# Optimization experiments

Hardware: AMD Instinct MI355X
Metric: run time of the kernel (lower is better)

The kernel has to match this reference:

```python
import jax, jax.numpy as jnp
import numpy as np
import math

N_HEADS = 8

def _bn_eval(x, g, b, m, v):
    # eval-mode BatchNorm over the last (query_size) axis, eps=1e-5 (torch default)
    return g * (x - m) * jax.lax.rsqrt(v + 1e-5) + b

def _forward(ht, k_proj_W, query, uk_W, u_q1W, u_q2, vhq, vhk, vcq, vck,
             k_proj_b, q_b, u_q1b, bnc_g, bnc_b, bnc_m, bnc_v, bnk_g, bnk_b, bnk_m, bnk_v):
    B, T, C = ht.shape
    N = N_HEADS
    D = C // N
    Q = k_proj_W.shape[-1]
    # contextual key: per-head [mean, std] over time (torch.std is unbiased)
    mean = jnp.mean(ht, axis=1)
    std = jnp.std(ht, axis=1, ddof=1)
    # cat on dim=2 of [B,C,1] then reshape -> interleaved [m0,s0,m1,s1,...]
    c = jnp.concatenate([mean[..., None], std[..., None]], axis=2).reshape(B, N, 2 * D)
    head_ck = jnp.einsum('bkl,klm->bkm', c, uk_W)                           # [B,N,Q]
    head_key = jnp.einsum('btkl,klm->btkm', ht.reshape(B, T, N, D), k_proj_W)  # [B,T,N,Q]
    value = ht.reshape(B, T, N, D)
    # contextual query
    cq = jnp.einsum('bkl,klm->bkm', c, u_q1W) + u_q1b                       # [B,N,Q]
    cq = jnp.tanh(_bn_eval(jax.nn.relu(cq), bnc_g, bnc_b, bnc_m, bnc_v))
    cq = jnp.einsum('bkm,kmn->bkn', cq, u_q2)                               # [B,N,A]
    # lambda gates
    lam_k = jax.nn.sigmoid(
        jnp.einsum('btkq,kq->btk', head_key, vhk[..., 0])
        + jnp.einsum('bkq,kq->bk', head_ck, vck[..., 0])[:, None, :]
    )[..., None]                                                            # [B,T,N,1]
    lam_q = jax.nn.sigmoid(
        jnp.einsum('kqa,kaq->k', query, vhq[..., 0])[None, :]
        + jnp.einsum('bka,kaq->bk', cq, vcq[..., 0])
    )[:, :, None, None]                                                     # [B,N,1,1]
    head_cq = (1.0 - lam_q) * query[None] + lam_q * cq[:, :, None, :]       # [B,N,Q,A]
    head_key = (1.0 - lam_k) * head_key + lam_k * head_ck[:, None]          # [B,T,N,Q]
    head_key = jnp.tanh(_bn_eval(jax.nn.relu(head_key + k_proj_b), bnk_g, bnk_b, bnk_m, bnk_v))
    scores = jnp.einsum('btkq,bkqa->btka', head_key, head_cq) / math.sqrt(Q) + q_b  # [B,T,N,A]
    p = jax.nn.softmax(scores, axis=1)                                      # softmax over time
    mu = jnp.sum(value * p, axis=1)                                         # [B,N,D] (A==D)
    rh = jnp.sqrt(jnp.clip(jnp.sum(value * value * p, axis=1) - mu * mu, 1e-9, None))
    return jnp.concatenate([mu, rh], axis=1).reshape(B, -1)                 # [B, 2*C]


def setup_inputs() -> dict:
    B, T, C = 16, 2000, 1536
    N, D, Q, A = 8, 192, 256, 192
    key = jax.random.key(0)
    ks = jax.random.split(key, 24)

    def xav(k, shape):
        fan = shape[-2] + shape[-1] if len(shape) >= 2 else shape[-1] + 1
        return jax.random.normal(k, shape, jnp.float32) * float(np.sqrt(2.0 / fan))

    return {
        'ht': jax.random.normal(ks[0], (B, T, C), jnp.float32),
        'k_proj_W': xav(ks[1], (N, D, Q)),
        'query': xav(ks[2], (N, Q, A)),
        'uk_W': xav(ks[3], (N, 2 * D, Q)),
        'u_q1W': xav(ks[4], (N, 2 * D, Q)),
        'u_q2': xav(ks[5], (N, Q, A)),
        'vhq': xav(ks[6], (N, A, Q, 1)),
        'vhk': xav(ks[7], (N, Q, 1)),
        'vcq': xav(ks[8], (N, A, Q, 1)),
        'vck': xav(ks[9], (N, Q, 1)),
        'k_proj_b': xav(ks[10], (N, Q)),
        'q_b': xav(ks[11], (N, A)),
        'u_q1b': xav(ks[12], (N, Q)),
        'bnc_g': jax.random.normal(ks[13], (Q,), jnp.float32) * 0.1 + 1.0,
        'bnc_b': jax.random.normal(ks[14], (Q,), jnp.float32) * 0.1,
        'bnc_m': jax.random.normal(ks[15], (Q,), jnp.float32) * 0.1,
        'bnc_v': jax.random.uniform(ks[16], (Q,), jnp.float32, 0.5, 1.5),
        'bnk_g': jax.random.normal(ks[17], (Q,), jnp.float32) * 0.1 + 1.0,
        'bnk_b': jax.random.normal(ks[18], (Q,), jnp.float32) * 0.1,
        'bnk_m': jax.random.normal(ks[19], (Q,), jnp.float32) * 0.1,
        'bnk_v': jax.random.uniform(ks[20], (Q,), jnp.float32, 0.5, 1.5),
    }


def reference(ht, k_proj_W, query, uk_W, u_q1W, u_q2, vhq, vhk, vcq, vck,
              k_proj_b, q_b, u_q1b, bnc_g, bnc_b, bnc_m, bnc_v, bnk_g, bnk_b, bnk_m, bnk_v):
    return _forward(ht, k_proj_W, query, uk_W, u_q1W, u_q2, vhq, vhk, vcq, vck,
                    k_proj_b, q_b, u_q1b, bnc_g, bnc_b, bnc_m, bnc_v,
                    bnk_g, bnk_b, bnk_m, bnk_v)
```

## Files before the change

kernel.cpp:

```cpp
#include <hip/hip_runtime.h>
#include <math.h>

#define BB 16
#define TT 2000
#define CC 1536
#define NH 8
#define DD 192
#define QQ 256
#define AA 192

#define WS_PSUM   0u
#define WS_PSQ    614400u
#define WS_CVEC   1228800u
#define WS_HCK    1277952u
#define WS_CKDOT  1310720u
#define WS_W1T    1310848u
#define WS_HCQT   1507456u
#define WS_PART   4653184u

#define LDS_BYTES 54272

typedef short bf16x8 __attribute__((ext_vector_type(8)));
typedef float f32x4  __attribute__((ext_vector_type(4)));

__device__ __forceinline__ float fast_tanh(float x) {
    return 1.f - 2.f / (__expf(2.f * x) + 1.f);
}
__device__ __forceinline__ float fast_sigmoid(float x) {
    return 1.f / (1.f + __expf(-x));
}
__device__ __forceinline__ short f2bf(float x) {
    unsigned u = __builtin_bit_cast(unsigned, x);
    u += 0x7FFFu + ((u >> 16) & 1u);
    return (short)(u >> 16);
}

__global__ void k_stats(const float* __restrict__ ht, float* __restrict__ ws) {
    int bid = blockIdx.x;
    int tc = bid % 25;
    int b  = bid / 25;
    int c4 = threadIdx.x * 4;
    const float* p = ht + ((size_t)b * TT + (size_t)tc * 80) * CC + c4;
    float4 s  = make_float4(0.f, 0.f, 0.f, 0.f);
    float4 s2 = make_float4(0.f, 0.f, 0.f, 0.f);
    #pragma unroll 8
    for (int i = 0; i < 80; ++i) {
        float4 v = *(const float4*)(p + (size_t)i * CC);
        s.x += v.x; s.y += v.y; s.z += v.z; s.w += v.w;
        s2.x = fmaf(v.x, v.x, s2.x); s2.y = fmaf(v.y, v.y, s2.y);
        s2.z = fmaf(v.z, v.z, s2.z); s2.w = fmaf(v.w, v.w, s2.w);
    }
    *(float4*)(ws + WS_PSUM + (size_t)(tc * BB + b) * CC + c4) = s;
    *(float4*)(ws + WS_PSQ  + (size_t)(tc * BB + b) * CC + c4) = s2;
}

__global__ void k_finstats(float* __restrict__ ws) {
    int b  = blockIdx.x;
    int c4 = threadIdx.x * 4;
    float4 s  = make_float4(0.f, 0.f, 0.f, 0.f);
    float4 s2 = make_float4(0.f, 0.f, 0.f, 0.f);
    for (int tc = 0; tc < 25; ++tc) {
        float4 a = *(const float4*)(ws + WS_PSUM + (size_t)(tc * BB + b) * CC + c4);
        float4 q = *(const float4*)(ws + WS_PSQ  + (size_t)(tc * BB + b) * CC + c4);
        s.x += a.x; s.y += a.y; s.z += a.z; s.w += a.w;
        s2.x += q.x; s2.y += q.y; s2.z += q.z; s2.w += q.w;
    }
    float mean[4] = {s.x, s.y, s.z, s.w};
    float sq[4]   = {s2.x, s2.y, s2.z, s2.w};
    float sd[4];
    #pragma unroll
    for (int j = 0; j < 4; ++j) {
        float m = mean[j] * (1.f / TT);
        float var = (sq[j] - (float)TT * m * m) * (1.f / (TT - 1));
        mean[j] = m;
        sd[j] = sqrtf(fmaxf(var, 0.f));
    }
    int k = c4 / DD, dd = c4 - k * DD;
    float* dst = ws + WS_CVEC + (size_t)b * 3072 + k * 384 + 2 * dd;
    *(float4*)(dst)     = make_float4(mean[0], sd[0], mean[1], sd[1]);
    *(float4*)(dst + 4) = make_float4(mean[2], sd[2], mean[3], sd[3]);
}

__global__ void k_convw(const float* __restrict__ kpW, float* __restrict__ ws) {
    int k  = blockIdx.x / 3, dc = blockIdx.x % 3;
    int q  = threadIdx.x;
    short* dst = (short*)(ws + WS_W1T) + ((size_t)k * QQ + q) * DD;
    const float* src = kpW + (size_t)k * DD * QQ + q;
    #pragma unroll 4
    for (int u = 0; u < 16; ++u) {
        int d = dc * 64 + u * 4;
        short4 s4;
        s4.x = f2bf(src[(size_t)(d + 0) * QQ]);
        s4.y = f2bf(src[(size_t)(d + 1) * QQ]);
        s4.z = f2bf(src[(size_t)(d + 2) * QQ]);
        s4.w = f2bf(src[(size_t)(d + 3) * QQ]);
        *(short4*)(dst + d) = s4;
    }
}

__global__ void k_prep(const float* __restrict__ ukW,  const float* __restrict__ uq1W,
                       const float* __restrict__ uq1b, const float* __restrict__ uq2,
                       const float* __restrict__ query, const float* __restrict__ vhq,
                       const float* __restrict__ vcq,  const float* __restrict__ vck,
                       const float* __restrict__ bncg, const float* __restrict__ bncb,
                       const float* __restrict__ bncm, const float* __restrict__ bncv,
                       float* __restrict__ ws) {
    __shared__ float cv[384];
    __shared__ float cqh[QQ];
    __shared__ float cq2s[AA];
    __shared__ float red[256];
    int bid = blockIdx.x;
    int b = bid >> 3, k = bid & 7;
    int tid = threadIdx.x;

    for (int i = tid; i < 384; i += 256)
        cv[i] = ws[WS_CVEC + (size_t)b * 3072 + k * 384 + i];
    __syncthreads();

    int q = tid;
    const float* up = ukW + (size_t)k * 384 * QQ;
    float hck = 0.f;
    for (int l = 0; l < 384; ++l) hck = fmaf(cv[l], up[l * QQ + q], hck);
    ws[WS_HCK + (size_t)(b * NH + k) * QQ + q] = hck;

    const float* u1 = uq1W + (size_t)k * 384 * QQ;
    float cq = uq1b[k * QQ + q];
    for (int l = 0; l < 384; ++l) cq = fmaf(cv[l], u1[l * QQ + q], cq);
    cq = fmaxf(cq, 0.f);
    float sc = bncg[q] * rsqrtf(bncv[q] + 1e-5f);
    cq = fast_tanh(fmaf(cq - bncm[q], sc, bncb[q]));
    cqh[q] = cq;

    red[tid] = hck * vck[k * QQ + q];
    __syncthreads();
    #pragma unroll
    for (int off = 128; off > 0; off >>= 1) {
        if (tid < off) red[tid] += red[tid + off];
        __syncthreads();
    }
    if (tid == 0) ws[WS_CKDOT + b * NH + k] = red[0];
    __syncthreads();

    float c2 = 0.f;
    if (tid < AA) {
        const float* u2 = uq2 + (size_t)k * QQ * AA + tid;
        for (int m = 0; m < QQ; ++m) c2 = fmaf(cqh[m], u2[m * AA], c2);
        cq2s[tid] = c2;
    }

    float part = 0.f;
    for (int idx = tid; idx < QQ * AA; idx += 256) {
        int qq = idx / AA, aa = idx - qq * AA;
        part = fmaf(query[(size_t)k * QQ * AA + idx],
                    vhq[(size_t)k * AA * QQ + aa * QQ + qq], part);
    }
    if (tid < AA) {
        const float* vq = vcq + (size_t)k * AA * QQ + (size_t)tid * QQ;
        float w = 0.f;
        for (int qx = 0; qx < QQ; ++qx) w += vq[qx];
        part = fmaf(c2, w, part);
    }
    red[tid] = part;
    __syncthreads();
    #pragma unroll
    for (int off = 128; off > 0; off >>= 1) {
        if (tid < off) red[tid] += red[tid + off];
        __syncthreads();
    }
    float lq = fast_sigmoid(red[0]);

    short* hq = (short*)(ws + WS_HCQT) + (size_t)(b * NH + k) * AA * QQ;
    const float* qr = query + (size_t)k * QQ * AA;
    for (int pos = tid; pos < AA * QQ; pos += 256) {
        int aa = pos >> 8, qq = pos & 255;
        float val = (1.f - lq) * qr[qq * AA + aa] + lq * cq2s[aa];
        hq[pos] = f2bf(val);
    }
}

__global__ __launch_bounds__(256, 3) void k_main(
        const float* __restrict__ ht,   const float* __restrict__ kpb,
        const float* __restrict__ vhk,  const float* __restrict__ qb_,
        const float* __restrict__ bnkg, const float* __restrict__ bnkb,
        const float* __restrict__ bnkm, const float* __restrict__ bnkv,
        float* __restrict__ ws) {
    extern __shared__ char lds[];
    float4* tbl4   = (float4*)(lds + 32768);
    float*  lamred = (float*)(lds + 36864);
    char*   Ab     = lds + 37888;
    float*  S_ld   = (float*)lds;

    int bid = blockIdx.x;
    int bk = bid >> 5, tile = bid & 31;
    int b = bk >> 3, k = bk & 7;
    int t0 = tile * 64;
    int tid = threadIdx.x;
    int w  = tid >> 6;
    int l  = tid & 63;
    int lr = l & 15, lg = l >> 4;
    int nv = min(64, TT - t0);

    {
        int q = tid;
        float hckv = ws[WS_HCK + (size_t)bk * QQ + q];
        float kbv  = kpb[k * QQ + q];
        float bscv = bnkg[q] * rsqrtf(bnkv[q] + 1e-5f);
        float bshv = bnkb[q] - bnkm[q] * bscv;
        tbl4[q] = make_float4(hckv, kbv, bscv, bshv);
    }
    float ckd = ws[WS_CKDOT + bk];

    float vv[4];
    #pragma unroll
    for (int cc = 0; cc < 4; ++cc)
        vv[cc] = vhk[k * QQ + w * 64 + cc * 16 + lr];

    f32x4 acc1[4][4];
    #pragma unroll
    for (int tg = 0; tg < 4; ++tg)
        #pragma unroll
        for (int cc = 0; cc < 4; ++cc) acc1[tg][cc] = (f32x4){0.f, 0.f, 0.f, 0.f};

    const short* w1s = (const short*)(ws + WS_W1T) + (size_t)k * QQ * DD;
    const int r_ = tid >> 2, cs = tid & 3;

    #pragma unroll
    for (int half = 0; half < 2; ++half) {
        __syncthreads();
        {
            const float* src = ht + ((size_t)b * TT + t0 + r_) * CC + k * DD + half * 96;
            bool ok = (t0 + r_) < TT;
            #pragma unroll
            for (int u = 0; u < 6; ++u) {
                int c4 = cs * 24 + u * 4;
                float4 v = make_float4(0.f, 0.f, 0.f, 0.f);
                if (ok) v = *(const float4*)(src + c4);
                short4 s4;
                s4.x = f2bf(v.x); s4.y = f2bf(v.y); s4.z = f2bf(v.z); s4.w = f2bf(v.w);
                int byte = (r_ << 8) + (c4 << 1);
                byte ^= (r_ & 7) << 4;
                *(short4*)(Ab + byte) = s4;
            }
        }
        __syncthreads();
        bf16x8 af[4][3];
        #pragma unroll
        for (int tg = 0; tg < 4; ++tg)
            #pragma unroll
            for (int kb = 0; kb < 3; ++kb) {
                int t = tg * 16 + lr;
                int byte = (t << 8) + ((kb * 32 + lg * 8) << 1);
                byte ^= (t & 7) << 4;
                af[tg][kb] = *(const bf16x8*)(Ab + byte);
            }
        #pragma unroll
        for (int cc = 0; cc < 4; ++cc) {
            const short* bq = w1s + (size_t)(w * 64 + cc * 16 + lr) * DD + half * 96 + lg * 8;
            bf16x8 bf0 = *(const bf16x8*)(bq);
            bf16x8 bf1 = *(const bf16x8*)(bq + 32);
            bf16x8 bf2 = *(const bf16x8*)(bq + 64);
            #pragma unroll
            for (int tg = 0; tg < 4; ++tg) {
                acc1[tg][cc] = __builtin_amdgcn_mfma_f32_16x16x32_bf16(af[tg][0], bf0, acc1[tg][cc], 0, 0, 0);
                acc1[tg][cc] = __builtin_amdgcn_mfma_f32_16x16x32_bf16(af[tg][1], bf1, acc1[tg][cc], 0, 0, 0);
                acc1[tg][cc] = __builtin_amdgcn_mfma_f32_16x16x32_bf16(af[tg][2], bf2, acc1[tg][cc], 0, 0, 0);
            }
        }
    }

    {
        float rdp[4][4];
        #pragma unroll
        for (int tg = 0; tg < 4; ++tg)
            #pragma unroll
            for (int r = 0; r < 4; ++r) {
                float s = 0.f;
                #pragma unroll
                for (int cc = 0; cc < 4; ++cc) s = fmaf(acc1[tg][cc][r], vv[cc], s);
                #pragma unroll
                for (int off = 1; off < 16; off <<= 1) s += __shfl_xor(s, off);
                rdp[tg][r] = s;
            }
        if (lr == 0) {
            #pragma unroll
            for (int tg = 0; tg < 4; ++tg)
                #pragma unroll
                for (int r = 0; r < 4; ++r)
                    lamred[w * 64 + tg * 16 + lg * 4 + r] = rdp[tg][r];
        }
    }
    __syncthreads();
    if (tid < 64) {
        float s = lamred[tid] + lamred[64 + tid] + lamred[128 + tid] + lamred[192 + tid];
        lamred[tid] = fast_sigmoid(s + ckd);
    }
    __syncthreads();

    {
        float lamv[4][4];
        #pragma unroll
        for (int tg = 0; tg < 4; ++tg)
            #pragma unroll
            for (int r = 0; r < 4; ++r)
                lamv[tg][r] = lamred[tg * 16 + lg * 4 + r];
        #pragma unroll
        for (int cc = 0; cc < 4; ++cc) {
            int q = w * 64 + cc * 16 + lr;
            float4 tv = tbl4[q];
            #pragma unroll
            for (int tg = 0; tg < 4; ++tg)
                #pragma unroll
                for (int r = 0; r < 4; ++r) {
                    float lam = lamv[tg][r];
                    float hk = (1.f - lam) * acc1[tg][cc][r] + lam * tv.x;
                    float x  = fmaxf(hk + tv.y, 0.f);
                    float kh = fast_tanh(fmaf(x, tv.z, tv.w));
                    int t = tg * 16 + lg * 4 + r;
                    int byte = (t << 9) + (q << 1);
                    byte ^= (t & 7) << 4;
                    *(short*)(lds + byte) = f2bf(kh);
                }
        }
    }
    __syncthreads();

    f32x4 acc2[4][3];
    #pragma unroll
    for (int tg = 0; tg < 4; ++tg)
        #pragma unroll
        for (int cc = 0; cc < 3; ++cc) acc2[tg][cc] = (f32x4){0.f, 0.f, 0.f, 0.f};

    const short* hq = (const short*)(ws + WS_HCQT) + (size_t)bk * AA * QQ;
    #pragma unroll
    for (int kb = 0; kb < 8; ++kb) {
        bf16x8 kf[4];
        #pragma unroll
        for (int tg = 0; tg < 4; ++tg) {
            int t = tg * 16 + lr;
            int byte = (t << 9) + ((kb * 32 + lg * 8) << 1);
            byte ^= (t & 7) << 4;
            kf[tg] = *(const bf16x8*)(lds + byte);
        }
        #pragma unroll
        for (int cc = 0; cc < 3; ++cc) {
            const short* ba = hq + (size_t)(w * 48 + cc * 16 + lr) * QQ + kb * 32 + lg * 8;
            bf16x8 bfv = *(const bf16x8*)ba;
            #pragma unroll
            for (int tg = 0; tg < 4; ++tg)
                acc2[tg][cc] = __builtin_amdgcn_mfma_f32_16x16x32_bf16(kf[tg], bfv, acc2[tg][cc], 0, 0, 0);
        }
    }
    __syncthreads();

    #pragma unroll
    for (int tg = 0; tg < 4; ++tg)
        #pragma unroll
        for (int cc = 0; cc < 3; ++cc) {
            int a = w * 48 + cc * 16 + lr;
            #pragma unroll
            for (int r = 0; r < 4; ++r)
                S_ld[(tg * 16 + lg * 4 + r) * 196 + a] = acc2[tg][cc][r];
        }
    __syncthreads();

    if (tid < AA) {
        int a = tid;
        float qb = qb_[k * AA + a];
        const float* vp = ht + ((size_t)b * TT + t0) * CC + k * DD + a;
        float lsum = 0.f, mac = 0.f, m2 = 0.f;
        if (nv == 64) {
            #pragma unroll 8
            for (int t = 0; t < 64; ++t) {
                float s = fminf(fmaf(S_ld[t * 196 + a], 0.0625f, qb), 30.f);
                float e = __expf(s);
                float v = vp[(size_t)t * CC];
                float t1 = e * v;
                lsum += e;
                mac  += t1;
                m2    = fmaf(t1, v, m2);
            }
        } else {
            for (int t = 0; t < nv; ++t) {
                float s = fminf(fmaf(S_ld[t * 196 + a], 0.0625f, qb), 30.f);
                float e = __expf(s);
                float v = vp[(size_t)t * CC];
                float t1 = e * v;
                lsum += e;
                mac  += t1;
                m2    = fmaf(t1, v, m2);
            }
        }
        ((float4*)(ws + WS_PART))[(size_t)(bk * 32 + tile) * AA + a] =
            make_float4(0.f, lsum, mac, m2);
    }
}

__global__ void k_merge(const float* __restrict__ ws, float* __restrict__ out) {
    int bk = blockIdx.x;
    int b = bk >> 3, k = bk & 7;
    int a = threadIdx.x;
    const float4* part = (const float4*)(ws + WS_PART) + (size_t)bk * 32 * AA + a;
    float M = -3.0e38f;
    #pragma unroll 4
    for (int ti = 0; ti < 32; ++ti) M = fmaxf(M, part[(size_t)ti * AA].x);
    float L = 0.f, MU = 0.f, M2 = 0.f;
    #pragma unroll 4
    for (int ti = 0; ti < 32; ++ti) {
        float4 p = part[(size_t)ti * AA];
        float sc = __expf(p.x - M);
        L  = fmaf(p.y, sc, L);
        MU = fmaf(p.z, sc, MU);
        M2 = fmaf(p.w, sc, M2);
    }
    MU /= L;
    M2 /= L;
    float rh = sqrtf(fmaxf(M2 - MU * MU, 1e-9f));
    out[(size_t)b * 3072 + k * DD + a]      = MU;
    out[(size_t)b * 3072 + CC + k * DD + a] = rh;
}

extern "C" void kernel_launch(void* const* d_in, const int* in_sizes, int n_in,
                              void* d_out, int out_size, void* d_ws, size_t ws_size,
                              hipStream_t stream) {
    const float* ht    = (const float*)d_in[0];
    const float* kpW   = (const float*)d_in[1];
    const float* query = (const float*)d_in[2];
    const float* ukW   = (const float*)d_in[3];
    const float* uq1W  = (const float*)d_in[4];
    const float* uq2   = (const float*)d_in[5];
    const float* vhq   = (const float*)d_in[6];
    const float* vhk   = (const float*)d_in[7];
    const float* vcq   = (const float*)d_in[8];
    const float* vck   = (const float*)d_in[9];
    const float* kpb   = (const float*)d_in[10];
    const float* qb    = (const float*)d_in[11];
    const float* uq1b  = (const float*)d_in[12];
    const float* bncg  = (const float*)d_in[13];
    const float* bncb  = (const float*)d_in[14];
    const float* bncm  = (const float*)d_in[15];
    const float* bncv  = (const float*)d_in[16];
    const float* bnkg  = (const float*)d_in[17];
    const float* bnkb  = (const float*)d_in[18];
    const float* bnkm  = (const float*)d_in[19];
    const float* bnkv  = (const float*)d_in[20];
    float* ws  = (float*)d_ws;
    float* out = (float*)d_out;

    hipFuncSetAttribute(reinterpret_cast<const void*>(k_main),
                        hipFuncAttributeMaxDynamicSharedMemorySize, LDS_BYTES);

    k_stats   <<<400, 384, 0, stream>>>(ht, ws);
    k_finstats<<<16, 384, 0, stream>>>(ws);
    k_convw   <<<24, 256, 0, stream>>>(kpW, ws);
    k_prep    <<<128, 256, 0, stream>>>(ukW, uq1W, uq1b, uq2, query, vhq, vcq, vck,
                                        bncg, bncb, bncm, bncv, ws);
    k_main    <<<4096, 256, LDS_BYTES, stream>>>(ht, kpb, vhk, qb,
                                                 bnkg, bnkb, bnkm, bnkv, ws);
    k_merge   <<<128, 192, 0, stream>>>(ws, out);
}
```

Baseline: 675.3 us.

## Fuse prep kernels, pre-swizzle MFMA operands, and run softmax epilogue from registers

Merges the stats, weight conversion and batch-independent query-dot work into one launch, and folds finstats into k_prep. Weight and head-query operands are stored in an MFMA fragment-ready layout so k_main can load them contiguously per lane. The score epilogue now reads the accumulators directly instead of staging scores through LDS, which cuts LDS to allow 4 blocks per CU. k_merge drops the unused max-rescale pass. The combined changes add code complexity and register pressure in k_main.

Result: faster. 598.8 us (-11.3%).

```diff
diff --git a/kernel.cpp b/kernel.cpp
--- a/kernel.cpp
+++ b/kernel.cpp
@@ -11,14 +11,15 @@
 
 #define WS_PSUM   0u
 #define WS_PSQ    614400u
-#define WS_CVEC   1228800u
-#define WS_HCK    1277952u
-#define WS_CKDOT  1310720u
-#define WS_W1T    1310848u
-#define WS_HCQT   1507456u
-#define WS_PART   4653184u
-
-#define LDS_BYTES 54272
+#define WS_HCK    1228800u
+#define WS_CKDOT  1261568u
+#define WS_W1T    1261696u
+#define WS_HCQT   1458304u
+#define WS_PART   4604032u
+#define WS_QVHQ   7749760u
+#define WS_VCQS   7749768u
+
+#define LDS_BYTES 37888
 
 typedef short bf16x8 __attribute__((ext_vector_type(8)));
 typedef float f32x4  __attribute__((ext_vector_type(4)));
@@ -35,97 +36,117 @@
     return (short)(u >> 16);
 }
 
-__global__ void k_stats(const float* __restrict__ ht, float* __restrict__ ws) {
-    int bid = blockIdx.x;
-    int tc = bid % 25;
-    int b  = bid / 25;
-    int c4 = threadIdx.x * 4;
-    const float* p = ht + ((size_t)b * TT + (size_t)tc * 80) * CC + c4;
-    float4 s  = make_float4(0.f, 0.f, 0.f, 0.f);
-    float4 s2 = make_float4(0.f, 0.f, 0.f, 0.f);
-    #pragma unroll 8
-    for (int i = 0; i < 80; ++i) {
-        float4 v = *(const float4*)(p + (size_t)i * CC);
-        s.x += v.x; s.y += v.y; s.z += v.z; s.w += v.w;
-        s2.x = fmaf(v.x, v.x, s2.x); s2.y = fmaf(v.y, v.y, s2.y);
-        s2.z = fmaf(v.z, v.z, s2.z); s2.w = fmaf(v.w, v.w, s2.w);
-    }
-    *(float4*)(ws + WS_PSUM + (size_t)(tc * BB + b) * CC + c4) = s;
-    *(float4*)(ws + WS_PSQ  + (size_t)(tc * BB + b) * CC + c4) = s2;
-}
-
-__global__ void k_finstats(float* __restrict__ ws) {
-    int b  = blockIdx.x;
-    int c4 = threadIdx.x * 4;
-    float4 s  = make_float4(0.f, 0.f, 0.f, 0.f);
-    float4 s2 = make_float4(0.f, 0.f, 0.f, 0.f);
-    for (int tc = 0; tc < 25; ++tc) {
-        float4 a = *(const float4*)(ws + WS_PSUM + (size_t)(tc * BB + b) * CC + c4);
-        float4 q = *(const float4*)(ws + WS_PSQ  + (size_t)(tc * BB + b) * CC + c4);
-        s.x += a.x; s.y += a.y; s.z += a.z; s.w += a.w;
-        s2.x += q.x; s2.y += q.y; s2.z += q.z; s2.w += q.w;
-    }
-    float mean[4] = {s.x, s.y, s.z, s.w};
-    float sq[4]   = {s2.x, s2.y, s2.z, s2.w};
-    float sd[4];
-    #pragma unroll
-    for (int j = 0; j < 4; ++j) {
-        float m = mean[j] * (1.f / TT);
-        float var = (sq[j] - (float)TT * m * m) * (1.f / (TT - 1));
-        mean[j] = m;
-        sd[j] = sqrtf(fmaxf(var, 0.f));
-    }
-    int k = c4 / DD, dd = c4 - k * DD;
-    float* dst = ws + WS_CVEC + (size_t)b * 3072 + k * 384 + 2 * dd;
-    *(float4*)(dst)     = make_float4(mean[0], sd[0], mean[1], sd[1]);
-    *(float4*)(dst + 4) = make_float4(mean[2], sd[2], mean[3], sd[3]);
-}
-
-__global__ void k_convw(const float* __restrict__ kpW, float* __restrict__ ws) {
-    int k  = blockIdx.x / 3, dc = blockIdx.x % 3;
-    int q  = threadIdx.x;
-    short* dst = (short*)(ws + WS_W1T) + ((size_t)k * QQ + q) * DD;
-    const float* src = kpW + (size_t)k * DD * QQ + q;
-    #pragma unroll 4
-    for (int u = 0; u < 16; ++u) {
-        int d = dc * 64 + u * 4;
-        short4 s4;
-        s4.x = f2bf(src[(size_t)(d + 0) * QQ]);
-        s4.y = f2bf(src[(size_t)(d + 1) * QQ]);
-        s4.z = f2bf(src[(size_t)(d + 2) * QQ]);
-        s4.w = f2bf(src[(size_t)(d + 3) * QQ]);
-        *(short4*)(dst + d) = s4;
+__global__ void k_pre(const float* __restrict__ ht,   const float* __restrict__ kpW,
+                      const float* __restrict__ query, const float* __restrict__ vhq,
+                      const float* __restrict__ vcq,  float* __restrict__ ws) {
+    int bid = blockIdx.x, tid = threadIdx.x;
+    if (bid < 400) {
+        int tc = bid % 25;
+        int b  = bid / 25;
+        int c4 = tid * 4;
+        const float* p = ht + ((size_t)b * TT + (size_t)tc * 80) * CC + c4;
+        float4 s  = make_float4(0.f, 0.f, 0.f, 0.f);
+        float4 s2 = make_float4(0.f, 0.f, 0.f, 0.f);
+        #pragma unroll 8
+        for (int i = 0; i < 80; ++i) {
+            float4 v = *(const float4*)(p + (size_t)i * CC);
+            s.x += v.x; s.y += v.y; s.z += v.z; s.w += v.w;
+            s2.x = fmaf(v.x, v.x, s2.x); s2.y = fmaf(v.y, v.y, s2.y);
+            s2.z = fmaf(v.z, v.z, s2.z); s2.w = fmaf(v.w, v.w, s2.w);
+        }
+        *(float4*)(ws + WS_PSUM + (size_t)(tc * BB + b) * CC + c4) = s;
+        *(float4*)(ws + WS_PSQ  + (size_t)(tc * BB + b) * CC + c4) = s2;
+    } else if (bid < 448) {
+        if (tid < 256) {
+            int kk  = (bid - 400) / 6, kbg = (bid - 400) % 6;
+            int qg  = tid >> 4, lr = tid & 15;
+            short* w1f = (short*)(ws + WS_W1T) + (size_t)kk * 49152;
+            const float* src = kpW + (size_t)kk * DD * QQ;
+            int q = qg * 16 + lr;
+            #pragma unroll
+            for (int lg = 0; lg < 4; ++lg) {
+                bf16x8 v8;
+                #pragma unroll
+                for (int e = 0; e < 8; ++e) {
+                    int d = kbg * 32 + lg * 8 + e;
+                    v8[e] = f2bf(src[(size_t)d * QQ + q]);
+                }
+                *(bf16x8*)(w1f + ((qg * 6 + kbg) * 512 + (lg * 16 + lr) * 8)) = v8;
+            }
+        }
+    } else {
+        int kk = bid - 448;
+        __shared__ float red6[6];
+        float qv = 0.f;
+        if (tid < 192) {
+            int aa = tid;
+            const float* qp = query + (size_t)kk * QQ * AA + aa;
+            const float* hp = vhq + (size_t)kk * AA * QQ + (size_t)aa * QQ;
+            const float* cp = vcq + (size_t)kk * AA * QQ + (size_t)aa * QQ;
+            float vs = 0.f;
+            #pragma unroll 4
+            for (int qq = 0; qq < QQ; ++qq) {
+                qv = fmaf(qp[(size_t)qq * AA], hp[qq], qv);
+                vs += cp[qq];
+            }
+            ws[WS_VCQS + kk * 192 + aa] = vs;
+        }
+        #pragma unroll
+        for (int off = 1; off < 64; off <<= 1) qv += __shfl_xor(qv, off);
+        if ((tid & 63) == 0) red6[tid >> 6] = qv;
+        __syncthreads();
+        if (tid == 0)
+            ws[WS_QVHQ + kk] = red6[0] + red6[1] + red6[2] + red6[3] + red6[4] + red6[5];
     }
 }
 
 __global__ void k_prep(const float* __restrict__ ukW,  const float* __restrict__ uq1W,
                        const float* __restrict__ uq1b, const float* __restrict__ uq2,
-                       const float* __restrict__ query, const float* __restrict__ vhq,
-                       const float* __restrict__ vcq,  const float* __restrict__ vck,
+                       const float* __restrict__ query, const float* __restrict__ vck,
                        const float* __restrict__ bncg, const float* __restrict__ bncb,
                        const float* __restrict__ bncm, const float* __restrict__ bncv,
                        float* __restrict__ ws) {
     __shared__ float cv[384];
     __shared__ float cqh[QQ];
-    __shared__ float cq2s[AA];
     __shared__ float red[256];
+    __shared__ float stage[32 * 196];
     int bid = blockIdx.x;
     int b = bid >> 3, k = bid & 7;
     int tid = threadIdx.x;
 
-    for (int i = tid; i < 384; i += 256)
-        cv[i] = ws[WS_CVEC + (size_t)b * 3072 + k * 384 + i];
+    if (tid < 192) {
+        float s = 0.f, s2 = 0.f;
+        #pragma unroll 5
+        for (int tc = 0; tc < 25; ++tc) {
+            s  += ws[WS_PSUM + (size_t)(tc * BB + b) * CC + k * DD + tid];
+            s2 += ws[WS_PSQ  + (size_t)(tc * BB + b) * CC + k * DD + tid];
+        }
+        float mean = s * (1.f / TT);
+        float var  = (s2 - (float)TT * mean * mean) * (1.f / (TT - 1));
+        cv[2 * tid]     = mean;
+        cv[2 * tid + 1] = sqrtf(fmaxf(var, 0.f));
+    }
     __syncthreads();
 
     int q = tid;
     const float* up = ukW + (size_t)k * 384 * QQ;
-    float hck = 0.f;
-    for (int l = 0; l < 384; ++l) hck = fmaf(cv[l], up[l * QQ + q], hck);
+    float hck = 0.f, hckb = 0.f;
+    #pragma unroll 4
+    for (int l = 0; l < 384; l += 2) {
+        hck  = fmaf(cv[l],     up[l * QQ + q],       hck);
+        hckb = fmaf(cv[l + 1], up[(l + 1) * QQ + q], hckb);
+    }
+    hck += hckb;
     ws[WS_HCK + (size_t)(b * NH + k) * QQ + q] = hck;
 
     const float* u1 = uq1W + (size_t)k * 384 * QQ;
-    float cq = uq1b[k * QQ + q];
-    for (int l = 0; l < 384; ++l) cq = fmaf(cv[l], u1[l * QQ + q], cq);
+    float cq = uq1b[k * QQ + q], cqb = 0.f;
+    #pragma unroll 4
+    for (int l = 0; l < 384; l += 2) {
+        cq  = fmaf(cv[l],     u1[l * QQ + q],       cq);
+        cqb = fmaf(cv[l + 1], u1[(l + 1) * QQ + q], cqb);
+    }
+    cq += cqb;
     cq = fmaxf(cq, 0.f);
     float sc = bncg[q] * rsqrtf(bncv[q] + 1e-5f);
     cq = fast_tanh(fmaf(cq - bncm[q], sc, bncb[q]));
@@ -144,41 +165,46 @@
     float c2 = 0.f;
     if (tid < AA) {
         const float* u2 = uq2 + (size_t)k * QQ * AA + tid;
+        #pragma unroll 4
         for (int m = 0; m < QQ; ++m) c2 = fmaf(cqh[m], u2[m * AA], c2);
-        cq2s[tid] = c2;
-    }
-
-    float part = 0.f;
-    for (int idx = tid; idx < QQ * AA; idx += 256) {
-        int qq = idx / AA, aa = idx - qq * AA;
-        part = fmaf(query[(size_t)k * QQ * AA + idx],
-                    vhq[(size_t)k * AA * QQ + aa * QQ + qq], part);
-    }
-    if (tid < AA) {
-        const float* vq = vcq + (size_t)k * AA * QQ + (size_t)tid * QQ;
-        float w = 0.f;
-        for (int qx = 0; qx < QQ; ++qx) w += vq[qx];
-        part = fmaf(c2, w, part);
-    }
-    red[tid] = part;
+    }
+
+    red[tid] = (tid < AA) ? c2 * ws[WS_VCQS + k * 192 + tid] : 0.f;
     __syncthreads();
     #pragma unroll
     for (int off = 128; off > 0; off >>= 1) {
         if (tid < off) red[tid] += red[tid + off];
         __syncthreads();
     }
-    float lq = fast_sigmoid(red[0]);
-
-    short* hq = (short*)(ws + WS_HCQT) + (size_t)(b * NH + k) * AA * QQ;
-    const float* qr = query + (size_t)k * QQ * AA;
-    for (int pos = tid; pos < AA * QQ; pos += 256) {
-        int aa = pos >> 8, qq = pos & 255;
-        float val = (1.f - lq) * qr[qq * AA + aa] + lq * cq2s[aa];
-        hq[pos] = f2bf(val);
-    }
-}
-
-__global__ __launch_bounds__(256, 3) void k_main(
+    float lq = fast_sigmoid(red[0] + ws[WS_QVHQ + k]);
+    float one_lq = 1.f - lq;
+
+    {
+        const float* qpan = query + (size_t)k * QQ * AA;
+        short* hqf = (short*)(ws + WS_HCQT) + (size_t)(b * NH + k) * 49152;
+        int ag = tid >> 4, lr = tid & 15;
+        for (int kb = 0; kb < 8; ++kb) {
+            __syncthreads();
+            for (int i = tid; i < 32 * 192; i += 256) {
+                int qt = i / 192, aa = i - qt * 192;
+                stage[qt * 196 + aa] = qpan[(size_t)(kb * 32 + qt) * AA + aa];
+            }
+            __syncthreads();
+            if (tid < AA) {
+                #pragma unroll
+                for (int lg = 0; lg < 4; ++lg) {
+                    bf16x8 v8;
+                    #pragma unroll
+                    for (int e = 0; e < 8; ++e)
+                        v8[e] = f2bf(fmaf(one_lq, stage[(lg * 8 + e) * 196 + tid], lq * c2));
+                    *(bf16x8*)(hqf + ((ag * 8 + kb) * 64 + lg * 16 + lr) * 8) = v8;
+                }
+            }
+        }
+    }
+}
+
+__global__ __launch_bounds__(256, 4) void k_main(
         const float* __restrict__ ht,   const float* __restrict__ kpb,
         const float* __restrict__ vhk,  const float* __restrict__ qb_,
         const float* __restrict__ bnkg, const float* __restrict__ bnkb,
@@ -187,17 +213,16 @@
     extern __shared__ char lds[];
     float4* tbl4   = (float4*)(lds + 32768);
     float*  lamred = (float*)(lds + 36864);
-    char*   Ab     = lds + 37888;
-    float*  S_ld   = (float*)lds;
+    char*   Ab     = lds;
 
     int bid = blockIdx.x;
     int bk = bid >> 5, tile = bid & 31;
     int b = bk >> 3, k = bk & 7;
     int t0 = tile * 64;
     int tid = threadIdx.x;
-    int w  = tid >> 6;
-    int l  = tid & 63;
-    int lr = l & 15, lg = l >> 4;
+    int w   = tid >> 6;
+    int lid = tid & 63;
+    int lr = lid & 15, lg = lid >> 4;
     int nv = min(64, TT - t0);
 
     {
@@ -209,7 +234,6 @@
         tbl4[q] = make_float4(hckv, kbv, bscv, bshv);
     }
     float ckd = ws[WS_CKDOT + bk];
-
     float vv[4];
     #pragma unroll
     for (int cc = 0; cc < 4; ++cc)
@@ -221,7 +245,7 @@
         #pragma unroll
         for (int cc = 0; cc < 4; ++cc) acc1[tg][cc] = (f32x4){0.f, 0.f, 0.f, 0.f};
 
-    const short* w1s = (const short*)(ws + WS_W1T) + (size_t)k * QQ * DD;
+    const short* w1f = (const short*)(ws + WS_W1T) + (size_t)k * 49152;
     const int r_ = tid >> 2, cs = tid & 3;
 
     #pragma unroll
@@ -243,28 +267,25 @@
             }
         }
         __syncthreads();
-        bf16x8 af[4][3];
-        #pragma unroll
-        for (int tg = 0; tg < 4; ++tg)
-            #pragma unroll
-            for (int kb = 0; kb < 3; ++kb) {
+        #pragma unroll
+        for (int kb = 0; kb < 3; ++kb) {
+            bf16x8 af[4];
+            #pragma unroll
+            for (int tg = 0; tg < 4; ++tg) {
                 int t = tg * 16 + lr;
                 int byte = (t << 8) + ((kb * 32 + lg * 8) << 1);
                 byte ^= (t & 7) << 4;
-                af[tg][kb] = *(const bf16x8*)(Ab + byte);
-            }
-        #pragma unroll
-        for (int cc = 0; cc < 4; ++cc) {
-            const short* bq = w1s + (size_t)(w * 64 + cc * 16 + lr) * DD + half * 96 + lg * 8;
-            bf16x8 bf0 = *(const bf16x8*)(bq);
-            bf16x8 bf1 = *(const bf16x8*)(bq + 32);
-            bf16x8 bf2 = *(const bf16x8*)(bq + 64);
-            #pragma unroll
-            for (int tg = 0; tg < 4; ++tg) {
-                acc1[tg][cc] = __builtin_amdgcn_mfma_f32_16x16x32_bf16(af[tg][0], bf0, acc1[tg][cc], 0, 0, 0);
-                acc1[tg][cc] = __builtin_amdgcn_mfma_f32_16x16x32_bf16(af[tg][1], bf1, acc1[tg][cc], 0, 0, 0);
-                acc1[tg][cc] = __builtin_amdgcn_mfma_f32_16x16x32_bf16(af[tg][2], bf2, acc1[tg][cc], 0, 0, 0);
-            }
+                af[tg] = *(const bf16x8*)(Ab + byte);
+            }
+            bf16x8 bf4[4];
+            #pragma unroll
+            for (int cc = 0; cc < 4; ++cc)
+                bf4[cc] = *(const bf16x8*)(w1f + (((w * 4 + cc) * 6 + half * 3 + kb) << 9) + (lid << 3));
+            #pragma unroll
+            for (int cc = 0; cc < 4; ++cc)
+                #pragma unroll
+                for (int tg = 0; tg < 4; ++tg)
+                    acc1[tg][cc] = __builtin_amdgcn_mfma_f32_16x16x32_bf16(af[tg], bf4[cc], acc1[tg][cc], 0, 0, 0);
         }
     }
 
@@ -330,7 +351,7 @@
         #pragma unroll
         for (int cc = 0; cc < 3; ++cc) acc2[tg][cc] = (f32x4){0.f, 0.f, 0.f, 0.f};
 
-    const short* hq = (const short*)(ws + WS_HCQT) + (size_t)bk * AA * QQ;
+    const short* hqf = (const short*)(ws + WS_HCQT) + (size_t)bk * 49152;
     #pragma unroll
     for (int kb = 0; kb < 8; ++kb) {
         bf16x8 kf[4];
@@ -341,57 +362,60 @@
             byte ^= (t & 7) << 4;
             kf[tg] = *(const bf16x8*)(lds + byte);
         }
-        #pragma unroll
-        for (int cc = 0; cc < 3; ++cc) {
-            const short* ba = hq + (size_t)(w * 48 + cc * 16 + lr) * QQ + kb * 32 + lg * 8;
-            bf16x8 bfv = *(const bf16x8*)ba;
+        bf16x8 bf3[3];
+        #pragma unroll
+        for (int cc = 0; cc < 3; ++cc)
+            bf3[cc] = *(const bf16x8*)(hqf + (((w * 3 + cc) * 8 + kb) << 9) + (lid << 3));
+        #pragma unroll
+        for (int cc = 0; cc < 3; ++cc)
             #pragma unroll
             for (int tg = 0; tg < 4; ++tg)
-                acc2[tg][cc] = __builtin_amdgcn_mfma_f32_16x16x32_bf16(kf[tg], bfv, acc2[tg][cc], 0, 0, 0);
-        }
-    }
-    __syncthreads();
-
-    #pragma unroll
-    for (int tg = 0; tg < 4; ++tg)
-        #pragma unroll
-        for (int cc = 0; cc < 3; ++cc) {
-            int a = w * 48 + cc * 16 + lr;
-            #pragma unroll
-            for (int r = 0; r < 4; ++r)
-                S_ld[(tg * 16 + lg * 4 + r) * 196 + a] = acc2[tg][cc][r];
-        }
-    __syncthreads();
-
-    if (tid < AA) {
-        int a = tid;
-        float qb = qb_[k * AA + a];
+                acc2[tg][cc] = __builtin_amdgcn_mfma_f32_16x16x32_bf16(kf[tg], bf3[cc], acc2[tg][cc], 0, 0, 0);
+    }
+
+    #pragma unroll
+    for (int cc = 0; cc < 3; ++cc) {
+        int a = w * 48 + cc * 16 + lr;
+        float qbv = qb_[k * AA + a];
         const float* vp = ht + ((size_t)b * TT + t0) * CC + k * DD + a;
         float lsum = 0.f, mac = 0.f, m2 = 0.f;
         if (nv == 64) {
-            #pragma unroll 8
-            for (int t = 0; t < 64; ++t) {
-                float s = fminf(fmaf(S_ld[t * 196 + a], 0.0625f, qb), 30.f);
-                float e = __expf(s);
-                float v = vp[(size_t)t * CC];
-                float t1 = e * v;
-                lsum += e;
-                mac  += t1;
-                m2    = fmaf(t1, v, m2);
-            }
+            #pragma unroll
+            for (int tg = 0; tg < 4; ++tg)
+                #pragma unroll
+                for (int r = 0; r < 4; ++r) {
+                    int t = tg * 16 + lg * 4 + r;
+                    float s = fminf(fmaf(acc2[tg][cc][r], 0.0625f, qbv), 30.f);
+                    float e = __expf(s);
+                    float v = vp[(size_t)t * CC];
+                    float t1 = e * v;
+                    lsum += e;
+                    mac  += t1;
+                    m2    = fmaf(t1, v, m2);
+                }
         } else {
-            for (int t = 0; t < nv; ++t) {
-                float s = fminf(fmaf(S_ld[t * 196 + a], 0.0625f, qb), 30.f);
-                float e = __expf(s);
-                float v = vp[(size_t)t * CC];
-                float t1 = e * v;
-                lsum += e;
-                mac  += t1;
-                m2    = fmaf(t1, v, m2);
-            }
-        }
-        ((float4*)(ws + WS_PART))[(size_t)(bk * 32 + tile) * AA + a] =
-            make_float4(0.f, lsum, mac, m2);
+            #pragma unroll
+            for (int tg = 0; tg < 4; ++tg)
+                #pragma unroll
+                for (int r = 0; r < 4; ++r) {
+                    int t = tg * 16 + lg * 4 + r;
+                    if (t < nv) {
+                        float s = fminf(fmaf(acc2[tg][cc][r], 0.0625f, qbv), 30.f);
+                        float e = __expf(s);
+                        float v = vp[(size_t)t * CC];
+                        float t1 = e * v;
+                        lsum += e;
+                        mac  += t1;
+                        m2    = fmaf(t1, v, m2);
+                    }
+                }
+        }
+        lsum += __shfl_xor(lsum, 16); lsum += __shfl_xor(lsum, 32);
+        mac  += __shfl_xor(mac, 16);  mac  += __shfl_xor(mac, 32);
+        m2   += __shfl_xor(m2, 16);   m2   += __shfl_xor(m2, 32);
+        if (lg == 0)
+            ((float4*)(ws + WS_PART))[(size_t)(bk * 32 + tile) * AA + a] =
+                make_float4(0.f, lsum, mac, m2);
     }
 }
 
@@ -400,17 +424,11 @@
     int b = bk >> 3, k = bk & 7;
     int a = threadIdx.x;
     const float4* part = (const float4*)(ws + WS_PART) + (size_t)bk * 32 * AA + a;
-    float M = -3.0e38f;
-    #pragma unroll 4
-    for (int ti = 0; ti < 32; ++ti) M = fmaxf(M, part[(size_t)ti * AA].x);
     float L = 0.f, MU = 0.f, M2 = 0.f;
-    #pragma unroll 4
+    #pragma unroll 8
     for (int ti = 0; ti < 32; ++ti) {
         float4 p = part[(size_t)ti * AA];
-        float sc = __expf(p.x - M);
-        L  = fmaf(p.y, sc, L);
-        MU = fmaf(p.z, sc, MU);
-        M2 = fmaf(p.w, sc, M2);
+        L += p.y; MU += p.z; M2 += p.w;
     }
     MU /= L;
     M2 /= L;
@@ -449,12 +467,10 @@
     hipFuncSetAttribute(reinterpret_cast<const void*>(k_main),
                         hipFuncAttributeMaxDynamicSharedMemorySize, LDS_BYTES);
 
-    k_stats   <<<400, 384, 0, stream>>>(ht, ws);
-    k_finstats<<<16, 384, 0, stream>>>(ws);
-    k_convw   <<<24, 256, 0, stream>>>(kpW, ws);
-    k_prep    <<<128, 256, 0, stream>>>(ukW, uq1W, uq1b, uq2, query, vhq, vcq, vck,
-                                        bncg, bncb, bncm, bncv, ws);
-    k_main    <<<4096, 256, LDS_BYTES, stream>>>(ht, kpb, vhk, qb,
-                                                 bnkg, bnkb, bnkm, bnkv, ws);
-    k_merge   <<<128, 192, 0, stream>>>(ws, out);
-}
+    k_pre  <<<456, 384, 0, stream>>>(ht, kpW, query, vhq, vcq, ws);
+    k_prep <<<128, 256, 0, stream>>>(ukW, uq1W, uq1b, uq2, query, vck,
+                                     bncg, bncb, bncm, bncv, ws);
+    k_main <<<4096, 256, LDS_BYTES, stream>>>(ht, kpb, vhk, qb,
+                                              bnkg, bnkb, bnkm, bnkv, ws);
+    k_merge<<<128, 192, 0, stream>>>(ws, out);
+}
```
